# Performance work log

Hardware: AMD Instinct MI355X
Metric: run time of the kernel (lower is better)

The kernel has to match this reference:

```python
import jax, jax.numpy as jnp
import numpy as np

DIM = 256
HEADS = 8
CAMS = 6
MINSIZE = 25  # AdaptiveAvgPool2d output size = min(feature_map_size)


def layernorm(x, g, b, eps=1e-5):
    mu = x.mean(-1, keepdims=True)
    var = ((x - mu) ** 2).mean(-1, keepdims=True)
    return (x - mu) / jnp.sqrt(var + eps) * g + b


def setup_inputs() -> dict:
    key = jax.random.key(0)
    ks = jax.random.split(key, 16)
    d, n = DIM, CAMS
    s = 0.02
    inp = {}
    inp["q"] = jax.random.normal(ks[0], (2, n, d, 50, 50), jnp.float32)
    inp["k"] = jax.random.normal(ks[1], (2, n, d, 50, 50), jnp.float32)
    inp["v"] = jax.random.normal(ks[2], (2, n, d, 50, 50), jnp.float32)
    inp["Wq"] = jax.random.normal(ks[3], (d, d), jnp.float32) * s
    inp["bq"] = jnp.zeros((d,), jnp.float32)
    inp["Wk"] = jax.random.normal(ks[4], (d, d), jnp.float32) * s
    inp["bk"] = jnp.zeros((d,), jnp.float32)
    inp["Wv"] = jax.random.normal(ks[5], (d, d), jnp.float32) * s
    inp["bv"] = jnp.zeros((d,), jnp.float32)
    inp["Wproj"] = jax.random.normal(ks[6], (n * d, d), jnp.float32) * s
    inp["bproj"] = jnp.zeros((d,), jnp.float32)
    inp["Waddq"] = jax.random.normal(ks[7], (n * d, d), jnp.float32) * s
    inp["baddq"] = jnp.zeros((d,), jnp.float32)
    inp["W1"] = jax.random.normal(ks[8], (d, 2 * d), jnp.float32) * s
    inp["b1"] = jnp.zeros((2 * d,), jnp.float32)
    inp["W2"] = jax.random.normal(ks[9], (2 * d, d), jnp.float32) * s
    inp["b2"] = jnp.zeros((d,), jnp.float32)
    inp["g_pre"] = jnp.ones((n * d,), jnp.float32)
    inp["b_pre"] = jnp.zeros((n * d,), jnp.float32)
    inp["g_norm"] = jnp.ones((d,), jnp.float32)
    inp["b_norm"] = jnp.zeros((d,), jnp.float32)
    return inp


def reference(q, k, v, Wq, bq, Wk, bk, Wv, bv, Wproj, bproj, Waddq, baddq,
              W1, b1, W2, b2, g_pre, b_pre, g_norm, b_norm):
    B, n, d, H, W = q.shape
    m = HEADS
    dh = d // m
    Q = H * W

    # residual query path: (b n d H W) -> (b HW (n d)) -> add_qproj -> (b HW d)
    add_q = jnp.transpose(q, (0, 3, 4, 1, 2)).reshape(B, Q, n * d) @ Waddq + baddq

    # queries: (b n d H W) -> (b n HW d) -> to_q
    qf = jnp.transpose(q, (0, 1, 3, 4, 2)).reshape(B, n, Q, d) @ Wq + bq

    # adaptive avg pool to MINSIZE (exact 2x2 bins since 50 = 2*25)
    def pool(t):
        _, _, _, h, w = t.shape
        return t.reshape(B, n, d, MINSIZE, h // MINSIZE, MINSIZE, w // MINSIZE).mean((4, 6))

    kp = pool(k)  # (b n d 25 25)
    vp = pool(v)
    K = MINSIZE * MINSIZE
    # (avg pool commutes with the pointwise linear to_k/to_v)
    kf = jnp.transpose(kp, (0, 1, 3, 4, 2)).reshape(B, n, K, d) @ Wk + bk
    vf = jnp.transpose(vp, (0, 1, 3, 4, 2)).reshape(B, n, K, d) @ Wv + bv

    # split heads
    qh = qf.reshape(B, n, Q, m, dh)
    kh = kf.reshape(B, n, K, m, dh)
    vh = vf.reshape(B, n, K, m, dh)

    # per-camera scores, softmax jointly over concatenated camera keys
    scores = (dh ** -0.5) * jnp.einsum('bnqmd,bnkmd->bmqnk', qh, kh)  # (B,m,Q,n,K)
    attn = jax.nn.softmax(scores.reshape(B, m, Q, n * K), axis=-1).reshape(B, m, Q, n, K)

    # per-camera attention output, concat cams (and heads within each cam) -> (B,Q,n*d)
    out = jnp.einsum('bmqnk,bnkmd->bqnmd', attn, vh).reshape(B, Q, n * d)

    x = layernorm(out, g_pre, b_pre) @ Wproj + bproj  # (B,Q,d)
    x = x + add_q
    h1 = jax.nn.gelu(x @ W1 + b1, approximate=False)
    x = x + layernorm(h1 @ W2 + b2, g_norm, b_norm)
    return jnp.transpose(x.reshape(B, H, W, d), (0, 3, 1, 2))  # (B,d,H,W)
```

## Files before the change

kernel.cpp:

```cpp
#include <hip/hip_runtime.h>
#include <math.h>

#define BATCH 2
#define NCAM 6
#define DIM 256
#define HEADS 8
#define DH 32
#define HW 2500
#define KP 625
#define NDIM (NCAM*DIM)

typedef __attribute__((ext_vector_type(8))) short short8;
typedef __attribute__((ext_vector_type(4))) short short4s;
typedef __attribute__((ext_vector_type(4))) float f32x4;

__device__ __forceinline__ short f2bf(float f) {
    union { float f; unsigned u; } v; v.f = f;
    unsigned r = v.u + 0x7fffu + ((v.u >> 16) & 1u);
    return (short)(r >> 16);
}
__device__ __forceinline__ float bf2f(short h) {
    union { unsigned u; float f; } v; v.u = ((unsigned)(unsigned short)h) << 16;
    return v.f;
}

struct WJ { const float* src; short* dst; int K, N; };
struct WArgs { WJ j[7]; };

__global__ __launch_bounds__(256) void prep_all(
    const float* __restrict__ q, const float* __restrict__ k,
    const float* __restrict__ v, short* __restrict__ qbf,
    short* __restrict__ kpbf, short* __restrict__ vpbf, WArgs wa)
{
    __shared__ float t[32][33];
    const int tx = threadIdx.x & 31, ty = threadIdx.x >> 5;
    int i = blockIdx.x;
    if (i < 7584) {
        int slab = i / 632, rem = i % 632;
        int hwB = (rem % 79) * 32, dB = (rem / 79) * 32;
        const float* src = q + (size_t)slab * 640000;
#pragma unroll
        for (int ii = 0; ii < 32; ii += 8) {
            int hw = hwB + tx;
            t[ty + ii][tx] = (hw < HW) ? src[(size_t)(dB + ty + ii) * HW + hw] : 0.f;
        }
        __syncthreads();
#pragma unroll
        for (int ii = 0; ii < 32; ii += 8) {
            int hw = hwB + ty + ii;
            if (hw < HW)
                qbf[((size_t)slab * HW + hw) * DIM + dB + tx] = f2bf(t[tx][ty + ii]);
        }
    } else if (i < 11424) {
        int i2 = i - 7584;
        const float* base; short* dst;
        if (i2 < 1920) { base = k; dst = kpbf; }
        else           { base = v; dst = vpbf; i2 -= 1920; }
        int slab = i2 / 160, rem = i2 % 160;
        int kpB = (rem % 20) * 32, dB = (rem / 20) * 32;
        const float* src = base + (size_t)slab * 640000;
        dst += (size_t)slab * (KP * DIM);
#pragma unroll
        for (int ii = 0; ii < 32; ii += 8) {
            int kp = kpB + tx;
            float val = 0.f;
            if (kp < KP) {
                int r2 = (kp / 25) * 2, c2 = (kp % 25) * 2;
                const float* p0 = src + (size_t)(dB + ty + ii) * HW + r2 * 50 + c2;
                val = 0.25f * (p0[0] + p0[1] + p0[50] + p0[51]);
            }
            t[ty + ii][tx] = val;
        }
        __syncthreads();
#pragma unroll
        for (int ii = 0; ii < 32; ii += 8) {
            int kp = kpB + ty + ii;
            if (kp < KP)
                dst[(size_t)kp * DIM + dB + tx] = f2bf(t[tx][ty + ii]);
        }
    } else {
        int wi = i - 11424;
        WJ jb = wa.j[0];
        for (int jj = 0; jj < 7; jj++) {
            jb = wa.j[jj];
            int cnt = (jb.K >> 5) * (jb.N >> 5);
            if (wi < cnt) break;
            wi -= cnt;
        }
        int tn = jb.N >> 5;
        int nB = (wi % tn) * 32, kB = (wi / tn) * 32;
#pragma unroll
        for (int ii = 0; ii < 32; ii += 8)
            t[ty + ii][tx] = jb.src[(size_t)(kB + ty + ii) * jb.N + nB + tx];
        __syncthreads();
#pragma unroll
        for (int ii = 0; ii < 32; ii += 8)
            jb.dst[(size_t)(nB + ty + ii) * jb.K + kB + tx] = f2bf(t[tx][ty + ii]);
    }
}

struct GJob { const short* A; const short* Bt; const float* bias;
              short* Cb; float* Cf; int M, K, yb, mode; };
struct GArgs { GJob j[4]; };

__global__ __launch_bounds__(256) void gemm_in(GArgs ga) {
    GJob jb = ga.j[blockIdx.z];
    if ((int)blockIdx.y >= jb.yb) return;
    __shared__ short As[128 * 32];
    __shared__ short Bs[64 * 32];

    const int tid  = threadIdx.x;
    const int nB   = blockIdx.x * 64;
    const int rB   = blockIdx.y * 128;
    const int w    = tid >> 6;
    const int lane = tid & 63;
    const int l15  = lane & 15;
    const int quad = lane >> 4;
    const int M = jb.M, K = jb.K;

    f32x4 acc[2][4];
#pragma unroll
    for (int i = 0; i < 2; i++)
#pragma unroll
        for (int jt = 0; jt < 4; jt++) acc[i][jt] = (f32x4){0.f, 0.f, 0.f, 0.f};

    const int ra = tid >> 1, k0 = (tid & 1) * 16;
    const int rga = rB + ra;
    const int bb = rga / 2500, hwp = rga % 2500;
    const int nb_ = tid >> 2, gkb = tid & 3;

    short8 pa0 = {0,0,0,0,0,0,0,0}, pa1 = pa0, pb = pa0;
    if (rga < M) {
        if (jb.mode) {
            int cam = k0 >> 8, c = k0 & 255;
            const short* p = &jb.A[(((size_t)(bb * 6 + cam)) * HW + hwp) * DIM + c];
            pa0 = *(const short8*)p; pa1 = *(const short8*)(p + 8);
        } else {
            const short* p = &jb.A[(size_t)rga * K + k0];
            pa0 = *(const short8*)p; pa1 = *(const short8*)(p + 8);
        }
    }
    pb = *(const short8*)&jb.Bt[(size_t)(nB + nb_) * K + gkb * 8];

    for (int kB = 0; kB < K; kB += 32) {
        __syncthreads();
        {
            int g0 = k0 >> 3;
            *(short8*)&As[ra * 32 + ((g0 ^ (ra & 3)) << 3)]       = pa0;
            *(short8*)&As[ra * 32 + (((g0 + 1) ^ (ra & 3)) << 3)] = pa1;
            *(short8*)&Bs[nb_ * 32 + ((gkb ^ (nb_ & 3)) << 3)]    = pb;
        }
        __syncthreads();
        int kN = kB + 32;
        if (kN < K) {
            if (rga < M) {
                if (jb.mode) {
                    int kk = kN + k0;
                    int cam = kk >> 8, c = kk & 255;
                    const short* p = &jb.A[(((size_t)(bb * 6 + cam)) * HW + hwp) * DIM + c];
                    pa0 = *(const short8*)p; pa1 = *(const short8*)(p + 8);
                } else {
                    const short* p = &jb.A[(size_t)rga * K + kN + k0];
                    pa0 = *(const short8*)p; pa1 = *(const short8*)(p + 8);
                }
            }
            pb = *(const short8*)&jb.Bt[(size_t)(nB + nb_) * K + kN + gkb * 8];
        }
        short8 af[2], bfr[4];
#pragma unroll
        for (int i = 0; i < 2; i++) {
            int m = w * 32 + i * 16 + l15;
            af[i] = *(const short8*)&As[m * 32 + ((quad ^ (m & 3)) << 3)];
        }
#pragma unroll
        for (int jt = 0; jt < 4; jt++) {
            int n = jt * 16 + l15;
            bfr[jt] = *(const short8*)&Bs[n * 32 + ((quad ^ (n & 3)) << 3)];
        }
#pragma unroll
        for (int i = 0; i < 2; i++)
#pragma unroll
            for (int jt = 0; jt < 4; jt++)
                acc[i][jt] = __builtin_amdgcn_mfma_f32_16x16x32_bf16(
                    af[i], bfr[jt], acc[i][jt], 0, 0, 0);
    }
#pragma unroll
    for (int i = 0; i < 2; i++) {
        int rbase = rB + w * 32 + i * 16 + quad * 4;
#pragma unroll
        for (int jt = 0; jt < 4; jt++) {
            int col = nB + jt * 16 + l15;
            float bcol = jb.bias[col];
#pragma unroll
            for (int reg = 0; reg < 4; reg++) {
                int rr = rbase + reg;
                if (rr < M) {
                    float vv = acc[i][jt][reg] + bcol;
                    if (jb.Cb) jb.Cb[(size_t)rr * 256 + col] = f2bf(vv);
                    else       jb.Cf[(size_t)rr * 256 + col] = vv;
                }
            }
        }
    }
}

template<int EPI, int WF32, int WBF>
__global__ __launch_bounds__(256) void mgemm_bf(
    const short* __restrict__ A, const short* __restrict__ Bt,
    const float* __restrict__ bias, const float* __restrict__ res,
    float* __restrict__ C, short* __restrict__ C2, int M, int N, int K)
{
    __shared__ short As[128 * 32];
    __shared__ short Bs[64 * 32];

    const int tid  = threadIdx.x;
    const int nB   = blockIdx.x * 64;
    const int rB   = blockIdx.y * 128;
    const int w    = tid >> 6;
    const int lane = tid & 63;
    const int l15  = lane & 15;
    const int quad = lane >> 4;

    f32x4 acc[2][4];
#pragma unroll
    for (int i = 0; i < 2; i++)
#pragma unroll
        for (int jt = 0; jt < 4; jt++) acc[i][jt] = (f32x4){0.f, 0.f, 0.f, 0.f};

    const int ra = tid >> 1, k0 = (tid & 1) * 16;
    const int rga = rB + ra;
    const int nb_ = tid >> 2, gkb = tid & 3;

    short8 pa0 = {0,0,0,0,0,0,0,0}, pa1 = pa0, pb = pa0;
    if (rga < M) {
        const short* p = &A[(size_t)rga * K + k0];
        pa0 = *(const short8*)p; pa1 = *(const short8*)(p + 8);
    }
    pb = *(const short8*)&Bt[(size_t)(nB + nb_) * K + gkb * 8];

    for (int kB = 0; kB < K; kB += 32) {
        __syncthreads();
        {
            int g0 = k0 >> 3;
            *(short8*)&As[ra * 32 + ((g0 ^ (ra & 3)) << 3)]       = pa0;
            *(short8*)&As[ra * 32 + (((g0 + 1) ^ (ra & 3)) << 3)] = pa1;
            *(short8*)&Bs[nb_ * 32 + ((gkb ^ (nb_ & 3)) << 3)]    = pb;
        }
        __syncthreads();
        int kN = kB + 32;
        if (kN < K) {
            if (rga < M) {
                const short* p = &A[(size_t)rga * K + kN + k0];
                pa0 = *(const short8*)p; pa1 = *(const short8*)(p + 8);
            }
            pb = *(const short8*)&Bt[(size_t)(nB + nb_) * K + kN + gkb * 8];
        }
        short8 af[2], bfr[4];
#pragma unroll
        for (int i = 0; i < 2; i++) {
            int m = w * 32 + i * 16 + l15;
            af[i] = *(const short8*)&As[m * 32 + ((quad ^ (m & 3)) << 3)];
        }
#pragma unroll
        for (int jt = 0; jt < 4; jt++) {
            int n = jt * 16 + l15;
            bfr[jt] = *(const short8*)&Bs[n * 32 + ((quad ^ (n & 3)) << 3)];
        }
#pragma unroll
        for (int i = 0; i < 2; i++)
#pragma unroll
            for (int jt = 0; jt < 4; jt++)
                acc[i][jt] = __builtin_amdgcn_mfma_f32_16x16x32_bf16(
                    af[i], bfr[jt], acc[i][jt], 0, 0, 0);
    }
#pragma unroll
    for (int i = 0; i < 2; i++) {
        int rbase = rB + w * 32 + i * 16 + quad * 4;
#pragma unroll
        for (int jt = 0; jt < 4; jt++) {
            int col = nB + jt * 16 + l15;
            float bcol = bias[col];
#pragma unroll
            for (int reg = 0; reg < 4; reg++) {
                int rr = rbase + reg;
                if (rr < M) {
                    float vv = acc[i][jt][reg] + bcol;
                    if (EPI == 1) vv = 0.5f * vv * (1.f + erff(vv * 0.70710678118654752f));
                    if (EPI == 2) vv += res[(size_t)rr * N + col];
                    if (WF32) C[(size_t)rr * N + col] = vv;
                    if (WBF)  C2[(size_t)rr * N + col] = f2bf(vv);
                }
            }
        }
    }
}

#define TQA 64
#define CH 64
#define VSTR 72

__global__ __launch_bounds__(256) void attn_mfma(
    const short* __restrict__ qf, const short* __restrict__ kf,
    const short* __restrict__ vf, short* __restrict__ attn_out,
    float* __restrict__ Zp)
{
    const int qt  = blockIdx.x;
    const int bm  = blockIdx.y;
    const int cam = blockIdx.z;
    const int b = bm >> 3, m = bm & 7;
    const int q0 = qt * TQA;
    const int tid = threadIdx.x;
    const int w = tid >> 6, lane = tid & 63;
    const int l15 = lane & 15, quad = lane >> 4;

    __shared__ __align__(16) short Ks[CH][DH];
    __shared__ __align__(16) short Vt[DH][VSTR];
    __shared__ __align__(16) short Pl[TQA][VSTR];

    const size_t slab = (size_t)(b * 6 + cam);

    int qrow = q0 + w * 16 + l15;
    int qcl  = qrow < HW ? qrow : HW - 1;
    const short8 aq = *(const short8*)&qf[(slab * HW + qcl) * DIM + m * DH + quad * 8];

    const short* kb = kf + slab * KP * DIM + m * DH;
    const short* vb = vf + slab * KP * DIM + m * DH;

    f32x4 oacc[2];
    oacc[0] = (f32x4){0.f, 0.f, 0.f, 0.f};
    oacc[1] = (f32x4){0.f, 0.f, 0.f, 0.f};
    float zp = 0.f;
    const float scale = 0.17677669529663687f;

    const int kl = tid >> 2, d8 = (tid & 3) * 8;
    const int kp2 = tid >> 3, dv = (tid & 7) * 4;
    const int vcol2 = (((kp2 >> 2) ^ (dv >> 3)) << 3) | ((2 * kp2) & 7);

    for (int c0 = 0; c0 < KP; c0 += CH) {
        __syncthreads();
        {
            int key = c0 + kl;
            short8 kv8 = {0, 0, 0, 0, 0, 0, 0, 0};
            if (key < KP) kv8 = *(const short8*)&kb[(size_t)key * DIM + d8];
            *(short8*)&Ks[kl][d8] = kv8;

            int k0v = c0 + 2 * kp2;
            short4s v0 = {0, 0, 0, 0}, v1 = {0, 0, 0, 0};
            if (k0v < KP)     v0 = *(const short4s*)&vb[(size_t)k0v * DIM + dv];
            if (k0v + 1 < KP) v1 = *(const short4s*)&vb[(size_t)(k0v + 1) * DIM + dv];
#pragma unroll
            for (int t = 0; t < 4; t++) {
                unsigned pk = (unsigned)(unsigned short)v0[t]
                            | ((unsigned)(unsigned short)v1[t] << 16);
                *(unsigned*)&Vt[dv + t][vcol2] = pk;
            }
        }
        __syncthreads();
        f32x4 sfragT[4];
#pragma unroll
        for (int jt = 0; jt < 4; jt++) {
            short8 bk8 = *(const short8*)&Ks[jt * 16 + l15][quad * 8];
            sfragT[jt] = __builtin_amdgcn_mfma_f32_16x16x32_bf16(
                bk8, aq, (f32x4){0.f, 0.f, 0.f, 0.f}, 0, 0, 0);
        }
        short* prow = &Pl[w * 16 + l15][0];
        if (c0 + CH <= KP) {
#pragma unroll
            for (int jt = 0; jt < 4; jt++) {
                float e0 = __expf(scale * sfragT[jt][0]);
                float e1 = __expf(scale * sfragT[jt][1]);
                float e2 = __expf(scale * sfragT[jt][2]);
                float e3 = __expf(scale * sfragT[jt][3]);
                zp += (e0 + e1) + (e2 + e3);
                unsigned lo, hi;
                asm("v_cvt_pk_bf16_f32 %0, %1, %2" : "=v"(lo) : "v"(e0), "v"(e1));
                asm("v_cvt_pk_bf16_f32 %0, %1, %2" : "=v"(hi) : "v"(e2), "v"(e3));
                unsigned long long pk64 = ((unsigned long long)hi << 32) | (unsigned long long)lo;
                *(unsigned long long*)&prow[jt * 16 + quad * 4] = pk64;
            }
        } else {
            int kbase = c0 + quad * 4;
#pragma unroll
            for (int jt = 0; jt < 4; jt++) {
                int kb0 = kbase + jt * 16;
                float e0 = (kb0 + 0 < KP) ? __expf(scale * sfragT[jt][0]) : 0.f;
                float e1 = (kb0 + 1 < KP) ? __expf(scale * sfragT[jt][1]) : 0.f;
                float e2 = (kb0 + 2 < KP) ? __expf(scale * sfragT[jt][2]) : 0.f;
                float e3 = (kb0 + 3 < KP) ? __expf(scale * sfragT[jt][3]) : 0.f;
                zp += (e0 + e1) + (e2 + e3);
                unsigned lo, hi;
                asm("v_cvt_pk_bf16_f32 %0, %1, %2" : "=v"(lo) : "v"(e0), "v"(e1));
                asm("v_cvt_pk_bf16_f32 %0, %1, %2" : "=v"(hi) : "v"(e2), "v"(e3));
                unsigned long long pk64 = ((unsigned long long)hi << 32) | (unsigned long long)lo;
                *(unsigned long long*)&prow[jt * 16 + quad * 4] = pk64;
            }
        }
#pragma unroll
        for (int ks = 0; ks < 2; ks++) {
            short8 ap = *(const short8*)&Pl[w * 16 + l15][ks * 32 + quad * 8];
#pragma unroll
            for (int nt = 0; nt < 2; nt++) {
                int dhn = nt * 16 + l15;
                int pgrp = ((ks * 4 + quad) ^ (dhn >> 3));
                short8 bv8 = *(const short8*)&Vt[dhn][pgrp << 3];
                oacc[nt] = __builtin_amdgcn_mfma_f32_16x16x32_bf16(
                    ap, bv8, oacc[nt], 0, 0, 0);
            }
        }
    }
    zp += __shfl_xor(zp, 16, 64);
    zp += __shfl_xor(zp, 32, 64);
    if (quad == 0) {
        int q = q0 + w * 16 + l15;
        if (q < HW) Zp[((size_t)bm * 6 + cam) * HW + q] = zp;
    }
#pragma unroll
    for (int reg = 0; reg < 4; reg++) {
        int q = q0 + w * 16 + quad * 4 + reg;
        if (q < HW) {
            size_t rowb = ((size_t)b * HW + q) * NDIM + cam * DIM + m * DH;
            attn_out[rowb + l15]      = f2bf(oacc[0][reg]);
            attn_out[rowb + 16 + l15] = f2bf(oacc[1][reg]);
        }
    }
}

__global__ __launch_bounds__(256) void ln_pre_kernel(
    const short* __restrict__ xin, short* __restrict__ lnbf,
    const float* __restrict__ Zp,
    const float* __restrict__ g, const float* __restrict__ bt)
{
    const int row = blockIdx.x;
    const int tid = threadIdx.x;
    const int b = row / 2500, q = row % 2500;
    __shared__ float zinv[8];
    if (tid < 8) {
        float z = 0.f;
#pragma unroll
        for (int cam = 0; cam < 6; cam++)
            z += Zp[((size_t)(b * 8 + tid) * 6 + cam) * HW + q];
        zinv[tid] = 1.f / z;
    }
    __syncthreads();
    const short* p = xin + (size_t)row * NDIM;
    float v[6];
    float s = 0.f, ss = 0.f;
#pragma unroll
    for (int i = 0; i < 6; i++) {
        int c = tid + i * 256;
        v[i] = bf2f(p[c]) * zinv[(c >> 5) & 7];
        s += v[i]; ss += v[i] * v[i];
    }
    __shared__ float rs[4], rss[4];
    int lane = tid & 63, wid = tid >> 6;
#pragma unroll
    for (int o = 32; o > 0; o >>= 1) { s += __shfl_down(s, o); ss += __shfl_down(ss, o); }
    if (lane == 0) { rs[wid] = s; rss[wid] = ss; }
    __syncthreads();
    s = rs[0] + rs[1] + rs[2] + rs[3];
    ss = rss[0] + rss[1] + rss[2] + rss[3];
    float mu = s * (1.f / NDIM);
    float var = ss * (1.f / NDIM) - mu * mu;
    float inv = rsqrtf(var + 1e-5f);
#pragma unroll
    for (int i = 0; i < 6; i++) {
        int c = tid + i * 256;
        lnbf[(size_t)row * NDIM + c] = f2bf((v[i] - mu) * inv * g[c] + bt[c]);
    }
}

__global__ __launch_bounds__(256) void final_kernel2(
    const float* __restrict__ x, const float* __restrict__ y2,
    const float* __restrict__ g, const float* __restrict__ bt,
    float* __restrict__ out)
{
    __shared__ float T[256][33];
    __shared__ float ps[32][8], pss[32][8];
    __shared__ float mu_s[32], inv_s[32];
    const int tid = threadIdx.x;
    const int rl = tid & 31, seg = tid >> 5;
    const int r0 = blockIdx.x * 32;
    const int row = r0 + rl;
    const bool ok = row < 5000;

    float4 yv[8];
    float s = 0.f, ss = 0.f;
    if (ok) {
        const float4* yp = (const float4*)(y2 + (size_t)row * DIM + seg * 32);
#pragma unroll
        for (int j = 0; j < 8; j++) {
            yv[j] = yp[j];
            s += yv[j].x + yv[j].y + yv[j].z + yv[j].w;
            ss += yv[j].x * yv[j].x + yv[j].y * yv[j].y
                + yv[j].z * yv[j].z + yv[j].w * yv[j].w;
        }
    } else {
#pragma unroll
        for (int j = 0; j < 8; j++) yv[j] = (float4){0, 0, 0, 0};
    }
    ps[rl][seg] = s; pss[rl][seg] = ss;
    __syncthreads();
    if (tid < 32) {
        float a = 0.f, b2 = 0.f;
#pragma unroll
        for (int j = 0; j < 8; j++) { a += ps[tid][j]; b2 += pss[tid][j]; }
        float mu = a * (1.f / DIM);
        float var = b2 * (1.f / DIM) - mu * mu;
        mu_s[tid] = mu;
        inv_s[tid] = rsqrtf(var + 1e-5f);
    }
    __syncthreads();
    if (ok) {
        float mu = mu_s[rl], inv = inv_s[rl];
        const float4* xp = (const float4*)(x + (size_t)row * DIM + seg * 32);
#pragma unroll
        for (int j = 0; j < 8; j++) {
            float4 xv = xp[j];
            int c = seg * 32 + j * 4;
            T[c + 0][rl] = xv.x + (yv[j].x - mu) * inv * g[c + 0] + bt[c + 0];
            T[c + 1][rl] = xv.y + (yv[j].y - mu) * inv * g[c + 1] + bt[c + 1];
            T[c + 2][rl] = xv.z + (yv[j].z - mu) * inv * g[c + 2] + bt[c + 2];
            T[c + 3][rl] = xv.w + (yv[j].w - mu) * inv * g[c + 3] + bt[c + 3];
        }
    }
    __syncthreads();
    const int w = tid >> 6, lane = tid & 63;
    const int hl = lane & 31, ch = lane >> 5;
    const int rr = r0 + hl;
    if (rr < 5000) {
        int b = rr / 2500, hw = rr % 2500;
        size_t obase = (size_t)b * 640000 + hw;
#pragma unroll
        for (int it = 0; it < 32; it++) {
            int c = it * 8 + w * 2 + ch;
            out[obase + (size_t)c * 2500] = T[c][hl];
        }
    }
}

extern "C" void kernel_launch(void* const* d_in, const int* in_sizes, int n_in,
                              void* d_out, int out_size, void* d_ws, size_t ws_size,
                              hipStream_t stream)
{
    const float* q     = (const float*)d_in[0];
    const float* k     = (const float*)d_in[1];
    const float* v     = (const float*)d_in[2];
    const float* Wq    = (const float*)d_in[3];
    const float* bq    = (const float*)d_in[4];
    const float* Wk    = (const float*)d_in[5];
    const float* bk    = (const float*)d_in[6];
    const float* Wv    = (const float*)d_in[7];
    const float* bv    = (const float*)d_in[8];
    const float* Wproj = (const float*)d_in[9];
    const float* bproj = (const float*)d_in[10];
    const float* Waddq = (const float*)d_in[11];
    const float* baddq = (const float*)d_in[12];
    const float* W1    = (const float*)d_in[13];
    const float* b1    = (const float*)d_in[14];
    const float* W2    = (const float*)d_in[15];
    const float* b2    = (const float*)d_in[16];
    const float* g_pre = (const float*)d_in[17];
    const float* b_pre = (const float*)d_in[18];
    const float* g_nrm = (const float*)d_in[19];
    const float* b_nrm = (const float*)d_in[20];
    float* out = (float*)d_out;

    float* ws = (float*)d_ws;
    short* qf_a   = (short*)(ws);
    short* lnbf   = (short*)(ws);
    short* qbf    = (short*)(ws + 3840000);
    short* kf_a   = (short*)(ws + 7680000);
    short* kpbf   = (short*)(ws + 8640000);
    short* vf_a   = (short*)(ws + 9600000);
    short* vpbf   = (short*)(ws + 10560000);
    float* add_q  = ws + 11520000;
    short* attn_o = (short*)(ws + 12800000);
    short* xbf    = (short*)(ws + 12800000);
    short* h1bf   = (short*)(ws + 13440000);
    float* x      = ws + 20480000;
    float* Zp     = ws + 21760000;
    short* eW     = (short*)(ws + 22000000);
    short* Wq_t    = eW;
    short* Wk_t    = eW + 65536;
    short* Wv_t    = eW + 131072;
    short* Waddq_t = eW + 196608;
    short* lW     = (short*)(ws + 22295000);
    short* Wproj_t = lW;
    short* W1_t    = lW + 393216;
    short* W2_t    = lW + 524288;
    float* y2     = ws + 22625000;

    dim3 blk(256);

    {
        WArgs wa;
        wa.j[0] = {Wq,    Wq_t,    256,  256};
        wa.j[1] = {Wk,    Wk_t,    256,  256};
        wa.j[2] = {Wv,    Wv_t,    256,  256};
        wa.j[3] = {Waddq, Waddq_t, 1536, 256};
        wa.j[4] = {Wproj, Wproj_t, 1536, 256};
        wa.j[5] = {W1,    W1_t,    256,  512};
        wa.j[6] = {W2,    W2_t,    512,  256};
        prep_all<<<dim3(12640), blk, 0, stream>>>(q, k, v, qbf, kpbf, vpbf, wa);
    }
    {
        GArgs ga;
        ga.j[0] = {qbf,  Wq_t,    bq,    qf_a, nullptr, 30000, 256,  235, 0};
        ga.j[1] = {kpbf, Wk_t,    bk,    kf_a, nullptr, 7500,  256,  59,  0};
        ga.j[2] = {vpbf, Wv_t,    bv,    vf_a, nullptr, 7500,  256,  59,  0};
        ga.j[3] = {qbf,  Waddq_t, baddq, nullptr, add_q, 5000, 1536, 40,  1};
        gemm_in<<<dim3(4, 235, 4), blk, 0, stream>>>(ga);
    }
    attn_mfma<<<dim3(40, 16, 6), blk, 0, stream>>>(qf_a, kf_a, vf_a, attn_o, Zp);
    ln_pre_kernel<<<dim3(5000), blk, 0, stream>>>(attn_o, lnbf, Zp, g_pre, b_pre);
    mgemm_bf<2, 1, 1><<<dim3(4, 40), blk, 0, stream>>>(
        lnbf, Wproj_t, bproj, add_q, x, xbf, 5000, 256, 1536);
    mgemm_bf<1, 0, 1><<<dim3(8, 40), blk, 0, stream>>>(
        xbf, W1_t, b1, nullptr, nullptr, h1bf, 5000, 512, 256);
    mgemm_bf<0, 1, 0><<<dim3(4, 40), blk, 0, stream>>>(
        h1bf, W2_t, b2, nullptr, y2, nullptr, 5000, 256, 512);
    final_kernel2<<<dim3(157), blk, 0, stream>>>(x, y2, g_nrm, b_nrm, out);
}
```

Baseline: 331.8 us.

## Keep attention probabilities in registers via permuted K layout and exp2 scaling

Permutes the order in which key rows are written into shared memory so the MFMA score output fragment matches the A-operand layout of the PV MFMA. The probabilities can then go straight from registers into the second MFMA, removing the Pl shared-memory round trip. The softmax scale times log2(e) is folded into the Q projection epilogue so the kernel can call the hardware exp2 directly, and the V transpose packing now uses byte-permute instructions. This adds index-mapping complexity and rounds the pre-scaled Q values to bf16.

New measurement: 323.0 us. 1.03x faster.

```diff
diff --git a/kernel.cpp b/kernel.cpp
--- a/kernel.cpp
+++ b/kernel.cpp
@@ -10,8 +10,9 @@
 #define KP 625
 #define NDIM (NCAM*DIM)
 
+#define SCALE_LOG2E 0.25503488494404f
+
 typedef __attribute__((ext_vector_type(8))) short short8;
-typedef __attribute__((ext_vector_type(4))) short short4s;
 typedef __attribute__((ext_vector_type(4))) float f32x4;
 
 __device__ __forceinline__ short f2bf(float f) {
@@ -22,6 +23,9 @@
 __device__ __forceinline__ float bf2f(short h) {
     union { unsigned u; float f; } v; v.u = ((unsigned)(unsigned short)h) << 16;
     return v.f;
+}
+__device__ __forceinline__ float exp2_hw(float x) {
+    return __builtin_amdgcn_exp2f(x);
 }
 
 struct WJ { const float* src; short* dst; int K, N; };
@@ -100,7 +104,7 @@
 }
 
 struct GJob { const short* A; const short* Bt; const float* bias;
-              short* Cb; float* Cf; int M, K, yb, mode; };
+              short* Cb; float* Cf; int M, K, yb, mode; float smul; };
 struct GArgs { GJob j[4]; };
 
 __global__ __launch_bounds__(256) void gemm_in(GArgs ga) {
@@ -195,7 +199,7 @@
             for (int reg = 0; reg < 4; reg++) {
                 int rr = rbase + reg;
                 if (rr < M) {
-                    float vv = acc[i][jt][reg] + bcol;
+                    float vv = (acc[i][jt][reg] + bcol) * jb.smul;
                     if (jb.Cb) jb.Cb[(size_t)rr * 256 + col] = f2bf(vv);
                     else       jb.Cf[(size_t)rr * 256 + col] = vv;
                 }
@@ -315,7 +319,6 @@
 
     __shared__ __align__(16) short Ks[CH][DH];
     __shared__ __align__(16) short Vt[DH][VSTR];
-    __shared__ __align__(16) short Pl[TQA][VSTR];
 
     const size_t slab = (size_t)(b * 6 + cam);
 
@@ -330,9 +333,11 @@
     oacc[0] = (f32x4){0.f, 0.f, 0.f, 0.f};
     oacc[1] = (f32x4){0.f, 0.f, 0.f, 0.f};
     float zp = 0.f;
-    const float scale = 0.17677669529663687f;
 
     const int kl = tid >> 2, d8 = (tid & 3) * 8;
+    const int jtw  = ((kl >> 5) & 1) | (((kl >> 2) & 1) << 1);
+    const int rw   = (((kl >> 3) & 3) << 2) | (kl & 3);
+    const int krow = jtw * 16 + rw;
     const int kp2 = tid >> 3, dv = (tid & 7) * 4;
     const int vcol2 = (((kp2 >> 2) ^ (dv >> 3)) << 3) | ((2 * kp2) & 7);
 
@@ -342,18 +347,16 @@
             int key = c0 + kl;
             short8 kv8 = {0, 0, 0, 0, 0, 0, 0, 0};
             if (key < KP) kv8 = *(const short8*)&kb[(size_t)key * DIM + d8];
-            *(short8*)&Ks[kl][d8] = kv8;
+            *(short8*)&Ks[krow][d8] = kv8;
 
             int k0v = c0 + 2 * kp2;
-            short4s v0 = {0, 0, 0, 0}, v1 = {0, 0, 0, 0};
-            if (k0v < KP)     v0 = *(const short4s*)&vb[(size_t)k0v * DIM + dv];
-            if (k0v + 1 < KP) v1 = *(const short4s*)&vb[(size_t)(k0v + 1) * DIM + dv];
-#pragma unroll
-            for (int t = 0; t < 4; t++) {
-                unsigned pk = (unsigned)(unsigned short)v0[t]
-                            | ((unsigned)(unsigned short)v1[t] << 16);
-                *(unsigned*)&Vt[dv + t][vcol2] = pk;
-            }
+            uint2 a0 = {0u, 0u}, a1 = {0u, 0u};
+            if (k0v < KP)     a0 = *(const uint2*)&vb[(size_t)k0v * DIM + dv];
+            if (k0v + 1 < KP) a1 = *(const uint2*)&vb[(size_t)(k0v + 1) * DIM + dv];
+            *(unsigned*)&Vt[dv + 0][vcol2] = __builtin_amdgcn_perm(a1.x, a0.x, 0x05040100u);
+            *(unsigned*)&Vt[dv + 1][vcol2] = __builtin_amdgcn_perm(a1.x, a0.x, 0x07060302u);
+            *(unsigned*)&Vt[dv + 2][vcol2] = __builtin_amdgcn_perm(a1.y, a0.y, 0x05040100u);
+            *(unsigned*)&Vt[dv + 3][vcol2] = __builtin_amdgcn_perm(a1.y, a0.y, 0x07060302u);
         }
         __syncthreads();
         f32x4 sfragT[4];
@@ -363,48 +366,45 @@
             sfragT[jt] = __builtin_amdgcn_mfma_f32_16x16x32_bf16(
                 bk8, aq, (f32x4){0.f, 0.f, 0.f, 0.f}, 0, 0, 0);
         }
-        short* prow = &Pl[w * 16 + l15][0];
+        union PA { unsigned u[4]; short8 s8; } pa[2];
         if (c0 + CH <= KP) {
 #pragma unroll
             for (int jt = 0; jt < 4; jt++) {
-                float e0 = __expf(scale * sfragT[jt][0]);
-                float e1 = __expf(scale * sfragT[jt][1]);
-                float e2 = __expf(scale * sfragT[jt][2]);
-                float e3 = __expf(scale * sfragT[jt][3]);
+                float e0 = exp2_hw(sfragT[jt][0]);
+                float e1 = exp2_hw(sfragT[jt][1]);
+                float e2 = exp2_hw(sfragT[jt][2]);
+                float e3 = exp2_hw(sfragT[jt][3]);
                 zp += (e0 + e1) + (e2 + e3);
-                unsigned lo, hi;
-                asm("v_cvt_pk_bf16_f32 %0, %1, %2" : "=v"(lo) : "v"(e0), "v"(e1));
-                asm("v_cvt_pk_bf16_f32 %0, %1, %2" : "=v"(hi) : "v"(e2), "v"(e3));
-                unsigned long long pk64 = ((unsigned long long)hi << 32) | (unsigned long long)lo;
-                *(unsigned long long*)&prow[jt * 16 + quad * 4] = pk64;
+                asm("v_cvt_pk_bf16_f32 %0, %1, %2"
+                    : "=v"(pa[jt & 1].u[(jt >> 1) * 2]) : "v"(e0), "v"(e1));
+                asm("v_cvt_pk_bf16_f32 %0, %1, %2"
+                    : "=v"(pa[jt & 1].u[(jt >> 1) * 2 + 1]) : "v"(e2), "v"(e3));
             }
         } else {
-            int kbase = c0 + quad * 4;
+            int kq8 = c0 + quad * 8;
 #pragma unroll
             for (int jt = 0; jt < 4; jt++) {
-                int kb0 = kbase + jt * 16;
-                float e0 = (kb0 + 0 < KP) ? __expf(scale * sfragT[jt][0]) : 0.f;
-                float e1 = (kb0 + 1 < KP) ? __expf(scale * sfragT[jt][1]) : 0.f;
-                float e2 = (kb0 + 2 < KP) ? __expf(scale * sfragT[jt][2]) : 0.f;
-                float e3 = (kb0 + 3 < KP) ? __expf(scale * sfragT[jt][3]) : 0.f;
+                int kb0 = kq8 + (jt & 1) * 32 + ((jt >> 1) << 2);
+                float e0 = (kb0 + 0 < KP) ? exp2_hw(sfragT[jt][0]) : 0.f;
+                float e1 = (kb0 + 1 < KP) ? exp2_hw(sfragT[jt][1]) : 0.f;
+                float e2 = (kb0 + 2 < KP) ? exp2_hw(sfragT[jt][2]) : 0.f;
+                float e3 = (kb0 + 3 < KP) ? exp2_hw(sfragT[jt][3]) : 0.f;
                 zp += (e0 + e1) + (e2 + e3);
-                unsigned lo, hi;
-                asm("v_cvt_pk_bf16_f32 %0, %1, %2" : "=v"(lo) : "v"(e0), "v"(e1));
-                asm("v_cvt_pk_bf16_f32 %0, %1, %2" : "=v"(hi) : "v"(e2), "v"(e3));
-                unsigned long long pk64 = ((unsigned long long)hi << 32) | (unsigned long long)lo;
-                *(unsigned long long*)&prow[jt * 16 + quad * 4] = pk64;
+                asm("v_cvt_pk_bf16_f32 %0, %1, %2"
+                    : "=v"(pa[jt & 1].u[(jt >> 1) * 2]) : "v"(e0), "v"(e1));
+                asm("v_cvt_pk_bf16_f32 %0, %1, %2"
+                    : "=v"(pa[jt & 1].u[(jt >> 1) * 2 + 1]) : "v"(e2), "v"(e3));
             }
         }
 #pragma unroll
         for (int ks = 0; ks < 2; ks++) {
-            short8 ap = *(const short8*)&Pl[w * 16 + l15][ks * 32 + quad * 8];
 #pragma unroll
             for (int nt = 0; nt < 2; nt++) {
                 int dhn = nt * 16 + l15;
                 int pgrp = ((ks * 4 + quad) ^ (dhn >> 3));
                 short8 bv8 = *(const short8*)&Vt[dhn][pgrp << 3];
                 oacc[nt] = __builtin_amdgcn_mfma_f32_16x16x32_bf16(
-                    ap, bv8, oacc[nt], 0, 0, 0);
+                    pa[ks].s8, bv8, oacc[nt], 0, 0, 0);
             }
         }
     }
@@ -605,10 +605,10 @@
     }
     {
         GArgs ga;
-        ga.j[0] = {qbf,  Wq_t,    bq,    qf_a, nullptr, 30000, 256,  235, 0};
-        ga.j[1] = {kpbf, Wk_t,    bk,    kf_a, nullptr, 7500,  256,  59,  0};
-        ga.j[2] = {vpbf, Wv_t,    bv,    vf_a, nullptr, 7500,  256,  59,  0};
-        ga.j[3] = {qbf,  Waddq_t, baddq, nullptr, add_q, 5000, 1536, 40,  1};
+        ga.j[0] = {qbf,  Wq_t,    bq,    qf_a, nullptr, 30000, 256,  235, 0, SCALE_LOG2E};
+        ga.j[1] = {kpbf, Wk_t,    bk,    kf_a, nullptr, 7500,  256,  59,  0, 1.0f};
+        ga.j[2] = {vpbf, Wv_t,    bv,    vf_a, nullptr, 7500,  256,  59,  0, 1.0f};
+        ga.j[3] = {qbf,  Waddq_t, baddq, nullptr, add_q, 5000, 1536, 40,  1, 1.0f};
         gemm_in<<<dim3(4, 235, 4), blk, 0, stream>>>(ga);
     }
     attn_mfma<<<dim3(40, 16, 6), blk, 0, stream>>>(qf_a, kf_a, vf_a, attn_o, Zp);
```
